# Optimization experiments

Measured on AMD Instinct MI355X. Metric: run time of the kernel, lower is better.

## Reference

```python
import jax, jax.numpy as jnp
import numpy as np

B, S, QD, KD, VD, OD = 8, 2048, 768, 768, 768, 512

def setup_inputs() -> dict:
    key = jax.random.key(0)
    ks = jax.random.split(key, 14)
    s_q = 1.0 / np.sqrt(QD)
    s_k = 1.0 / np.sqrt(KD)
    s_v = 1.0 / np.sqrt(VD)
    return {
        "query": jax.random.normal(ks[0], (B, S, QD), jnp.float32),
        "key": jax.random.normal(ks[1], (B, S, KD), jnp.float32),
        "value": jax.random.normal(ks[2], (B, S, VD), jnp.float32),
        "Wqr": jax.random.normal(ks[3], (QD, OD), jnp.float32) * s_q,
        "bqr": jnp.zeros((OD,), jnp.float32),
        "Wqi": jax.random.normal(ks[4], (QD, OD), jnp.float32) * s_q,
        "bqi": jnp.zeros((OD,), jnp.float32),
        "Wkr": jax.random.normal(ks[5], (KD, OD), jnp.float32) * s_k,
        "bkr": jnp.zeros((OD,), jnp.float32),
        "Wki": jax.random.normal(ks[6], (KD, OD), jnp.float32) * s_k,
        "bki": jnp.zeros((OD,), jnp.float32),
        "Wv": jax.random.normal(ks[7], (VD, OD), jnp.float32) * s_v,
        "bv": jnp.zeros((OD,), jnp.float32),
        "coherence_weight": jnp.asarray(1.0, jnp.float32),
    }

def reference(query, key, value, Wqr, bqr, Wqi, bqi, Wkr, bkr, Wki, bki, Wv, bv, coherence_weight):
    # Complex-valued projections (real/imag parts via separate linears)
    q_r = jnp.einsum("bsq,qo->bso", query, Wqr) + bqr
    q_i = jnp.einsum("bsq,qo->bso", query, Wqi) + bqi
    k_r = jnp.einsum("bsk,ko->bso", key, Wkr) + bkr
    k_i = jnp.einsum("bsk,ko->bso", key, Wki) + bki
    v = jnp.einsum("bsv,vo->bso", value, Wv) + bv
    # Complex QK^T: (q_r + i q_i)(k_r - i k_i)^T pieces, as in the torch code
    att_real = jnp.einsum("bso,bto->bst", q_r, k_r) + jnp.einsum("bso,bto->bst", q_i, k_i)
    att_imag = jnp.einsum("bso,bto->bst", q_i, k_r) - jnp.einsum("bso,bto->bst", q_r, k_i)
    att_mag = jnp.sqrt(att_real ** 2 + att_imag ** 2)
    scale = jnp.asarray(1.0 / np.sqrt(OD), att_mag.dtype)
    weights = jax.nn.softmax(att_mag * scale, axis=-1)  # [B,S,S]
    output = jnp.einsum("bst,bto->bso", weights, v)  # [B,S,OD]
    coherence = jnp.mean(att_imag ** 2) * coherence_weight
    return output, coherence
```

## Files before the change

### kernel.cpp

```cpp
#include <hip/hip_runtime.h>
#include <math.h>
#include <stdint.h>

#define S_    2048
#define SCALE_ 0.044194173824159216f

typedef __attribute__((ext_vector_type(8))) short short8;
typedef __attribute__((ext_vector_type(4))) float f32x4;

#define MFMA16(a, b, c) __builtin_amdgcn_mfma_f32_16x16x32_bf16((a), (b), (c), 0, 0, 0)

__device__ __forceinline__ void glds16(const void* g, void* l) {
  __builtin_amdgcn_global_load_lds(
      (const __attribute__((address_space(1))) void*)g,
      (__attribute__((address_space(3))) void*)l, 16, 0, 0);
}

__device__ __forceinline__ unsigned short f2bf(float f) {
  unsigned u = __float_as_uint(f);
  u += 0x7FFFu + ((u >> 16) & 1u);
  return (unsigned short)(u >> 16);
}

__global__ __launch_bounds__(256) void convert_kernel(
    const float* __restrict__ src, unsigned short* __restrict__ dst, int n4) {
  int i = blockIdx.x * 256 + threadIdx.x;
  if (i >= n4) return;
  float4 v = ((const float4*)src)[i];
  ushort4 o;
  o.x = f2bf(v.x); o.y = f2bf(v.y); o.z = f2bf(v.z); o.w = f2bf(v.w);
  ((ushort4*)dst)[i] = o;
}

__global__ void bias_build_kernel(const float* bqr, const float* bqi,
                                  const float* bkr, const float* bki,
                                  const float* bv, float* bq, float* bk,
                                  float* bvo) {
  int t = blockIdx.x * 256 + threadIdx.x;
  if (t < 512) { bq[t] = bqr[t]; bk[t] = bkr[t]; bvo[t] = bv[t]; }
  else if (t < 1024) { bq[t] = bqi[t - 512]; bk[t] = bki[t - 512]; }
}

__global__ __launch_bounds__(256) void wtrans_kernel(
    const float* __restrict__ W, unsigned short* __restrict__ Wt, int N,
    int row_off) {
  __shared__ float t[32][33];
  int n0 = blockIdx.x * 32, k0 = blockIdx.y * 32;
  int tx = threadIdx.x & 31, ty = threadIdx.x >> 5;
#pragma unroll
  for (int r = 0; r < 4; ++r)
    t[ty + r * 8][tx] = W[(size_t)(k0 + ty + r * 8) * N + n0 + tx];
  __syncthreads();
#pragma unroll
  for (int r = 0; r < 4; ++r)
    Wt[(size_t)(row_off + n0 + ty + r * 8) * 768 + k0 + tx] =
        f2bf(t[tx][ty + r * 8]);
}

__global__ void init_kernel(float* lsum, float* coh) {
  int t = blockIdx.x * 256 + threadIdx.x;
  if (t < 16384) lsum[t] = 0.f;
  if (t == 0) *coh = 0.f;
}

__global__ __launch_bounds__(256, 2) void proj_kernel(
    const unsigned short* __restrict__ Xb, const unsigned short* __restrict__ Wt,
    const float* __restrict__ bias, unsigned short* __restrict__ Y, int N,
    int vt_mode) {
  __shared__ char lds[32768];
  const int tid = threadIdx.x;
  const int lane = tid & 63, wid = tid >> 6;
  const int wi = wid >> 1, wj = wid & 1;
  const int m0 = blockIdx.y * 128, n0 = blockIdx.x * 128;
  const char* Xc = (const char*)Xb;
  const char* Wc = (const char*)Wt;

  f32x4 acc[4][4] = {};
  const int tile = wid >> 1;

  for (int s = 0; s < 12; ++s) {
    __syncthreads();
#pragma unroll
    for (int iss = 0; iss < 8; ++iss) {
      int gbase = wid * 512 + iss * 64;
      int loc = (gbase & 1023) + lane;
      int r = loc >> 3, blk = loc & 7;
      int sb = blk ^ (r & 7);
      const char* src = (tile == 0)
          ? Xc + (size_t)(m0 + r) * 1536 + s * 128 + sb * 16
          : Wc + (size_t)(n0 + r) * 1536 + s * 128 + sb * 16;
      glds16(src, lds + gbase * 16);
    }
    __syncthreads();
#pragma unroll
    for (int kk = 0; kk < 2; ++kk) {
      int blk = kk * 4 + (lane >> 4);
      short8 a[4];
#pragma unroll
      for (int i = 0; i < 4; ++i) {
        int row = wi * 64 + i * 16 + (lane & 15);
        a[i] = *(const short8*)(lds + row * 128 + ((blk ^ (row & 7)) << 4));
      }
#pragma unroll
      for (int j = 0; j < 4; ++j) {
        int row = wj * 64 + j * 16 + (lane & 15);
        short8 b = *(const short8*)(lds + 16384 + row * 128 +
                                    ((blk ^ (row & 7)) << 4));
#pragma unroll
        for (int i = 0; i < 4; ++i) acc[i][j] = MFMA16(a[i], b, acc[i][j]);
      }
    }
  }

#pragma unroll
  for (int j = 0; j < 4; ++j) {
    int n = n0 + wj * 64 + j * 16 + (lane & 15);
    float bn = bias[n];
    if (!vt_mode) {
#pragma unroll
      for (int i = 0; i < 4; ++i) {
        int mrow = m0 + wi * 64 + i * 16 + (lane >> 4) * 4;
#pragma unroll
        for (int r = 0; r < 4; ++r)
          Y[(size_t)(mrow + r) * N + n] = f2bf(acc[i][j][r] + bn);
      }
    } else {
#pragma unroll
      for (int i = 0; i < 4; ++i) {
        int mrow = m0 + wi * 64 + i * 16 + (lane >> 4) * 4;
        int b = mrow >> 11, key = mrow & 2047;
        ushort4 o;
        o.x = f2bf(acc[i][j][0] + bn);
        o.y = f2bf(acc[i][j][1] + bn);
        o.z = f2bf(acc[i][j][2] + bn);
        o.w = f2bf(acc[i][j][3] + bn);
        *(ushort4*)&Y[((size_t)b * 512 + n) * 2048 + key] = o;
      }
    }
  }
}

__global__ __launch_bounds__(256, 2) void score_kernel(
    const unsigned short* __restrict__ Qcat,
    const unsigned short* __restrict__ Kcat, unsigned short* __restrict__ P,
    float* __restrict__ lsum, float* __restrict__ coh) {
  __shared__ char lds[65536];
  const int tid = threadIdx.x;
  const int lane = tid & 63, wid = tid >> 6;
  const int wi = wid >> 1, wj = wid & 1;

  int id = blockIdx.x;
  int w = (id & 7) * 256 + (id >> 3);
  int batch = w >> 8;
  int tilein = w & 255;
  int q0 = (tilein >> 4) * 128;
  int k0 = (tilein & 15) * 128;

  const char* Qc = (const char*)Qcat + ((size_t)batch * 2048 + q0) * 2048;
  const char* Kc = (const char*)Kcat + ((size_t)batch * 2048 + k0) * 2048;

  f32x4 accre[4][4] = {}, accim[4][4] = {};
  const short sg = (short)0x8000;
  const short8 SGN = {sg, sg, sg, sg, sg, sg, sg, sg};

  const char* base = (wid < 2) ? Qc : Kc;
  const int hioff = (wid & 1) * 1024;

  for (int s = 0; s < 8; ++s) {
    __syncthreads();
#pragma unroll
    for (int iss = 0; iss < 16; ++iss) {
      int loc = iss * 64 + lane;
      int r = loc >> 3, blk = loc & 7;
      int sb = blk ^ (r & 7);
      glds16(base + (size_t)r * 2048 + s * 128 + hioff + sb * 16,
             lds + wid * 16384 + iss * 1024);
    }
    __syncthreads();
#pragma unroll
    for (int kk = 0; kk < 2; ++kk) {
      int blk = kk * 4 + (lane >> 4);
      short8 alo[4], ahi[4];
#pragma unroll
      for (int i = 0; i < 4; ++i) {
        int row = wi * 64 + i * 16 + (lane & 15);
        int sw = (blk ^ (row & 7)) << 4;
        alo[i] = *(const short8*)(lds + row * 128 + sw);
        ahi[i] = *(const short8*)(lds + 16384 + row * 128 + sw);
      }
#pragma unroll
      for (int j = 0; j < 4; ++j) {
        int row = wj * 64 + j * 16 + (lane & 15);
        int sw = (blk ^ (row & 7)) << 4;
        short8 blo = *(const short8*)(lds + 32768 + row * 128 + sw);
        short8 bhi = *(const short8*)(lds + 49152 + row * 128 + sw);
        short8 bhin = bhi ^ SGN;
#pragma unroll
        for (int i = 0; i < 4; ++i) {
          accre[i][j] = MFMA16(alo[i], blo, accre[i][j]);
          accre[i][j] = MFMA16(ahi[i], bhi, accre[i][j]);
          accim[i][j] = MFMA16(ahi[i], blo, accim[i][j]);
          accim[i][j] = MFMA16(alo[i], bhin, accim[i][j]);
        }
      }
    }
  }

  float csum = 0.f;
  size_t prow_base = (size_t)batch * 2048;
  float rsum[16];
#pragma unroll
  for (int t = 0; t < 16; ++t) rsum[t] = 0.f;

#pragma unroll
  for (int i = 0; i < 4; ++i) {
#pragma unroll
    for (int r = 0; r < 4; ++r) {
      int row = q0 + wi * 64 + i * 16 + (lane >> 4) * 4 + r;
      unsigned short* prow = P + (prow_base + row) * 2048;
      float rs = 0.f;
#pragma unroll
      for (int j = 0; j < 4; ++j) {
        float re = accre[i][j][r], im = accim[i][j][r];
        csum += im * im;
        float p = __expf(sqrtf(re * re + im * im) * SCALE_);
        rs += p;
        prow[k0 + wj * 64 + j * 16 + (lane & 15)] = f2bf(p);
      }
      rsum[i * 4 + r] = rs;
    }
  }
#pragma unroll
  for (int t = 0; t < 16; ++t) {
    float v = rsum[t];
    v += __shfl_xor(v, 1, 64);
    v += __shfl_xor(v, 2, 64);
    v += __shfl_xor(v, 4, 64);
    v += __shfl_xor(v, 8, 64);
    rsum[t] = v;
  }
  if ((lane & 15) == 0) {
#pragma unroll
    for (int i = 0; i < 4; ++i)
#pragma unroll
      for (int r = 0; r < 4; ++r) {
        int row = q0 + wi * 64 + i * 16 + (lane >> 4) * 4 + r;
        atomicAdd(&lsum[prow_base + row], rsum[i * 4 + r]);
      }
  }
#pragma unroll
  for (int m = 1; m < 64; m <<= 1) csum += __shfl_xor(csum, m, 64);
  __syncthreads();
  float* cred = (float*)lds;
  if (lane == 0) cred[wid] = csum;
  __syncthreads();
  if (tid == 0) atomicAdd(coh, cred[0] + cred[1] + cred[2] + cred[3]);
}

__global__ __launch_bounds__(256, 2) void pv_kernel(
    const unsigned short* __restrict__ P, const unsigned short* __restrict__ Vt,
    const float* __restrict__ lsum, float* __restrict__ out) {
  __shared__ char lds[32768];
  const int tid = threadIdx.x;
  const int lane = tid & 63, wid = tid >> 6;
  const int wi = wid >> 1, wj = wid & 1;

  int id = blockIdx.x;
  int w = (id & 7) * 64 + (id >> 3);
  int batch = w >> 6, tilein = w & 63;
  int i0 = (tilein >> 2) * 128;
  int o0 = (tilein & 3) * 128;

  const char* Pc = (const char*)P + (size_t)batch * 2048 * 4096;
  const char* Vc = (const char*)Vt + (size_t)batch * 512 * 4096;

  f32x4 acc[4][4] = {};
  const int tile = wid >> 1;

  for (int s = 0; s < 32; ++s) {
    __syncthreads();
#pragma unroll
    for (int iss = 0; iss < 8; ++iss) {
      int gbase = wid * 512 + iss * 64;
      int loc = (gbase & 1023) + lane;
      int r = loc >> 3, blk = loc & 7;
      int sb = blk ^ (r & 7);
      const char* src = (tile == 0)
          ? Pc + (size_t)(i0 + r) * 4096 + s * 128 + sb * 16
          : Vc + (size_t)(o0 + r) * 4096 + s * 128 + sb * 16;
      glds16(src, lds + gbase * 16);
    }
    __syncthreads();
#pragma unroll
    for (int kk = 0; kk < 2; ++kk) {
      int blk = kk * 4 + (lane >> 4);
      short8 a[4];
#pragma unroll
      for (int i = 0; i < 4; ++i) {
        int row = wi * 64 + i * 16 + (lane & 15);
        a[i] = *(const short8*)(lds + row * 128 + ((blk ^ (row & 7)) << 4));
      }
#pragma unroll
      for (int j = 0; j < 4; ++j) {
        int row = wj * 64 + j * 16 + (lane & 15);
        short8 b = *(const short8*)(lds + 16384 + row * 128 +
                                    ((blk ^ (row & 7)) << 4));
#pragma unroll
        for (int i = 0; i < 4; ++i) acc[i][j] = MFMA16(a[i], b, acc[i][j]);
      }
    }
  }

#pragma unroll
  for (int i = 0; i < 4; ++i) {
    int mrow = i0 + wi * 64 + i * 16 + (lane >> 4) * 4;
    float linv[4];
#pragma unroll
    for (int r = 0; r < 4; ++r)
      linv[r] = 1.0f / lsum[(size_t)batch * 2048 + mrow + r];
#pragma unroll
    for (int j = 0; j < 4; ++j) {
      int n = o0 + wj * 64 + j * 16 + (lane & 15);
#pragma unroll
      for (int r = 0; r < 4; ++r)
        out[((size_t)batch * 2048 + mrow + r) * 512 + n] = acc[i][j][r] * linv[r];
    }
  }
}

__global__ void finalize_kernel(const float* __restrict__ coh,
                                const float* __restrict__ cw,
                                float* __restrict__ out_last) {
  *out_last = (*coh) * (1.0f / 33554432.0f) * (*cw);
}

extern "C" void kernel_launch(void* const* d_in, const int* in_sizes, int n_in,
                              void* d_out, int out_size, void* d_ws,
                              size_t ws_size, hipStream_t stream) {
  const float* query = (const float*)d_in[0];
  const float* key   = (const float*)d_in[1];
  const float* value = (const float*)d_in[2];
  const float* Wqr = (const float*)d_in[3];
  const float* bqr = (const float*)d_in[4];
  const float* Wqi = (const float*)d_in[5];
  const float* bqi = (const float*)d_in[6];
  const float* Wkr = (const float*)d_in[7];
  const float* bkr = (const float*)d_in[8];
  const float* Wki = (const float*)d_in[9];
  const float* bki = (const float*)d_in[10];
  const float* Wv  = (const float*)d_in[11];
  const float* bv  = (const float*)d_in[12];
  const float* cw  = (const float*)d_in[13];
  float* out = (float*)d_out;

  char* ws = (char*)d_ws;
  unsigned short* XQ   = (unsigned short*)(ws + 0);
  unsigned short* XK   = (unsigned short*)(ws + 25165824);
  unsigned short* XV   = (unsigned short*)(ws + 50331648);
  unsigned short* Pbuf = (unsigned short*)(ws + 0);
  unsigned short* WTQ  = (unsigned short*)(ws + 75497472);
  unsigned short* WTK  = (unsigned short*)(ws + 77070336);
  unsigned short* WTV  = (unsigned short*)(ws + 78643200);
  float* BQ   = (float*)(ws + 79429632);
  float* BK   = (float*)(ws + 79433728);
  float* BV   = (float*)(ws + 79437824);
  unsigned short* QCAT = (unsigned short*)(ws + 79441920);
  unsigned short* KCAT = (unsigned short*)(ws + 112996352);
  unsigned short* VT   = (unsigned short*)(ws + 146550784);
  float* LSUM = (float*)(ws + 163328000);
  float* COH  = (float*)(ws + 163393536);
  if (ws_size < 163393600) return;

  convert_kernel<<<12288, 256, 0, stream>>>(query, XQ, 3145728);
  convert_kernel<<<12288, 256, 0, stream>>>(key, XK, 3145728);
  convert_kernel<<<12288, 256, 0, stream>>>(value, XV, 3145728);
  bias_build_kernel<<<4, 256, 0, stream>>>(bqr, bqi, bkr, bki, bv, BQ, BK, BV);
  wtrans_kernel<<<dim3(16, 24), 256, 0, stream>>>(Wqr, WTQ, 512, 0);
  wtrans_kernel<<<dim3(16, 24), 256, 0, stream>>>(Wqi, WTQ, 512, 512);
  wtrans_kernel<<<dim3(16, 24), 256, 0, stream>>>(Wkr, WTK, 512, 0);
  wtrans_kernel<<<dim3(16, 24), 256, 0, stream>>>(Wki, WTK, 512, 512);
  wtrans_kernel<<<dim3(16, 24), 256, 0, stream>>>(Wv, WTV, 512, 0);

  proj_kernel<<<dim3(8, 128), 256, 0, stream>>>(XQ, WTQ, BQ, QCAT, 1024, 0);
  proj_kernel<<<dim3(8, 128), 256, 0, stream>>>(XK, WTK, BK, KCAT, 1024, 0);
  proj_kernel<<<dim3(4, 128), 256, 0, stream>>>(XV, WTV, BV, VT, 512, 1);

  init_kernel<<<64, 256, 0, stream>>>(LSUM, COH);
  score_kernel<<<2048, 256, 0, stream>>>(QCAT, KCAT, Pbuf, LSUM, COH);
  pv_kernel<<<512, 256, 0, stream>>>(Pbuf, VT, LSUM, out);
  finalize_kernel<<<1, 1, 0, stream>>>(COH, cw, out + 8388608);
}
```

Measured before the change: 378.0 us.

## Pipeline score kernel with triple-buffered LDS, larger tiles, and fuse input converts

The score kernel moves to 512-thread blocks computing 256x128 tiles, with a three-stage LDS ring that prefetches K-slices two steps ahead. The prefetch loads are interleaved with the MFMA work, using explicit waitcnt, barriers and setprio. This targets the load/compute serialization of the old two-barrier loop and increases Q/K reuse per block. The three fp32-to-bf16 convert launches are merged into one. The cost is 144KB of LDS per block, which limits occupancy to one block per CU, plus more complex synchronization.

```diff
diff --git a/kernel.cpp b/kernel.cpp
--- a/kernel.cpp
+++ b/kernel.cpp
@@ -22,14 +22,19 @@
   return (unsigned short)(u >> 16);
 }
 
-__global__ __launch_bounds__(256) void convert_kernel(
-    const float* __restrict__ src, unsigned short* __restrict__ dst, int n4) {
+__global__ __launch_bounds__(256) void convert3_kernel(
+    const float* __restrict__ a, const float* __restrict__ b,
+    const float* __restrict__ c, unsigned short* __restrict__ oa,
+    unsigned short* __restrict__ ob, unsigned short* __restrict__ oc) {
   int i = blockIdx.x * 256 + threadIdx.x;
-  if (i >= n4) return;
-  float4 v = ((const float4*)src)[i];
+  int which = i / 3145728;
+  int off = i - which * 3145728;
+  const float* s = (which == 0) ? a : (which == 1) ? b : c;
+  unsigned short* d = (which == 0) ? oa : (which == 1) ? ob : oc;
+  float4 v = ((const float4*)s)[off];
   ushort4 o;
   o.x = f2bf(v.x); o.y = f2bf(v.y); o.z = f2bf(v.z); o.w = f2bf(v.w);
-  ((ushort4*)dst)[i] = o;
+  ((ushort4*)d)[off] = o;
 }
 
 __global__ void bias_build_kernel(const float* bqr, const float* bqi,
@@ -140,21 +145,24 @@
   }
 }
 
-__global__ __launch_bounds__(256, 2) void score_kernel(
+__global__ __launch_bounds__(512, 2) void score_kernel(
     const unsigned short* __restrict__ Qcat,
     const unsigned short* __restrict__ Kcat, unsigned short* __restrict__ P,
     float* __restrict__ lsum, float* __restrict__ coh) {
-  __shared__ char lds[65536];
+  __shared__ char lds[147456];
   const int tid = threadIdx.x;
   const int lane = tid & 63, wid = tid >> 6;
-  const int wi = wid >> 1, wj = wid & 1;
-
-  int id = blockIdx.x;
-  int w = (id & 7) * 256 + (id >> 3);
-  int batch = w >> 8;
-  int tilein = w & 255;
-  int q0 = (tilein >> 4) * 128;
-  int k0 = (tilein & 15) * 128;
+  const int wm = wid >> 1;
+  const int wn = wid & 1;
+  const int lr = lane & 15;
+  const int lk = lane >> 4;
+  const int l8 = lane >> 3, lb = lane & 7;
+
+  const int id = blockIdx.x;
+  const int batch = id & 7;
+  const int tile = id >> 3;
+  const int q0 = (tile >> 4) << 8;
+  const int k0 = (tile & 15) << 7;
 
   const char* Qc = (const char*)Qcat + ((size_t)batch * 2048 + q0) * 2048;
   const char* Kc = (const char*)Kcat + ((size_t)batch * 2048 + k0) * 2048;
@@ -163,60 +171,86 @@
   const short sg = (short)0x8000;
   const short8 SGN = {sg, sg, sg, sg, sg, sg, sg, sg};
 
-  const char* base = (wid < 2) ? Qc : Kc;
-  const int hioff = (wid & 1) * 1024;
-
-  for (int s = 0; s < 8; ++s) {
-    __syncthreads();
-#pragma unroll
-    for (int iss = 0; iss < 16; ++iss) {
-      int loc = iss * 64 + lane;
-      int r = loc >> 3, blk = loc & 7;
-      int sb = blk ^ (r & 7);
-      glds16(base + (size_t)r * 2048 + s * 128 + hioff + sb * 16,
-             lds + wid * 16384 + iss * 1024);
-    }
-    __syncthreads();
-#pragma unroll
-    for (int kk = 0; kk < 2; ++kk) {
-      int blk = kk * 4 + (lane >> 4);
-      short8 alo[4], ahi[4];
+  auto stage = [&](int t, char* setbase, int L) {
+    int row, sb;
+    const char* src;
+    if (L < 32) {
+      row = (L << 3) + l8;
+      sb = lb ^ (row & 7);
+      src = Qc + (size_t)row * 2048 + t * 64 + (sb & 3) * 16 + (sb >> 2) * 1024;
+    } else {
+      row = ((L - 32) << 3) + l8;
+      sb = lb ^ (row & 7);
+      src = Kc + (size_t)row * 2048 + t * 64 + (sb & 3) * 16 + (sb >> 2) * 1024;
+    }
+    glds16(src, setbase + (L << 10));
+  };
+
+#pragma unroll
+  for (int u = 0; u < 6; ++u) stage(0, lds, wid * 6 + u);
+#pragma unroll
+  for (int u = 0; u < 6; ++u) stage(1, lds + 49152, wid * 6 + u);
+  asm volatile("s_waitcnt vmcnt(6)" ::: "memory");
+  __builtin_amdgcn_s_barrier();
+
+  for (int t = 0; t < 16; ++t) {
+    char* rbase = lds + (t % 3) * 49152;
+    char* wbase = lds + ((t + 2) % 3) * 49152;
+    short8 alo[4], ahi[4];
+#pragma unroll
+    for (int j = 0; j < 4; ++j) {
+      if (j == 0) {
+#pragma unroll
+        for (int i = 0; i < 4; ++i) {
+          int ar = wm * 64 + i * 16 + lr;
+          const char* arow = rbase + ar * 128;
+          alo[i] = *(const short8*)(arow + ((lk ^ (ar & 7)) << 4));
+          ahi[i] = *(const short8*)(arow + (((4 + lk) ^ (ar & 7)) << 4));
+        }
+      }
+      int br = wn * 64 + j * 16 + lr;
+      const char* brow = rbase + 32768 + br * 128;
+      short8 blo = *(const short8*)(brow + ((lk ^ (br & 7)) << 4));
+      short8 bhi = *(const short8*)(brow + (((4 + lk) ^ (br & 7)) << 4));
+      if (t < 14) {
+        if (j == 0)      { stage(t + 2, wbase, wid * 6 + 0); stage(t + 2, wbase, wid * 6 + 1); }
+        else if (j == 1) { stage(t + 2, wbase, wid * 6 + 2); stage(t + 2, wbase, wid * 6 + 3); }
+        else if (j == 2) { stage(t + 2, wbase, wid * 6 + 4); }
+        else             { stage(t + 2, wbase, wid * 6 + 5); }
+      }
+      __builtin_amdgcn_s_barrier();
+      asm volatile("s_waitcnt lgkmcnt(0)" ::: "memory");
+      __builtin_amdgcn_sched_barrier(0);
+      __builtin_amdgcn_s_setprio(1);
+      short8 bhin = bhi ^ SGN;
 #pragma unroll
       for (int i = 0; i < 4; ++i) {
-        int row = wi * 64 + i * 16 + (lane & 15);
-        int sw = (blk ^ (row & 7)) << 4;
-        alo[i] = *(const short8*)(lds + row * 128 + sw);
-        ahi[i] = *(const short8*)(lds + 16384 + row * 128 + sw);
-      }
-#pragma unroll
-      for (int j = 0; j < 4; ++j) {
-        int row = wj * 64 + j * 16 + (lane & 15);
-        int sw = (blk ^ (row & 7)) << 4;
-        short8 blo = *(const short8*)(lds + 32768 + row * 128 + sw);
-        short8 bhi = *(const short8*)(lds + 49152 + row * 128 + sw);
-        short8 bhin = bhi ^ SGN;
-#pragma unroll
-        for (int i = 0; i < 4; ++i) {
-          accre[i][j] = MFMA16(alo[i], blo, accre[i][j]);
-          accre[i][j] = MFMA16(ahi[i], bhi, accre[i][j]);
-          accim[i][j] = MFMA16(ahi[i], blo, accim[i][j]);
-          accim[i][j] = MFMA16(alo[i], bhin, accim[i][j]);
-        }
-      }
-    }
-  }
+        accre[i][j] = MFMA16(alo[i], blo, accre[i][j]);
+        accre[i][j] = MFMA16(ahi[i], bhi, accre[i][j]);
+        accim[i][j] = MFMA16(ahi[i], blo, accim[i][j]);
+        accim[i][j] = MFMA16(alo[i], bhin, accim[i][j]);
+      }
+      __builtin_amdgcn_s_setprio(0);
+      if (j == 3) {
+        if (t < 14)       asm volatile("s_waitcnt vmcnt(6)" ::: "memory");
+        else if (t == 14) asm volatile("s_waitcnt vmcnt(0)" ::: "memory");
+      }
+      __builtin_amdgcn_s_barrier();
+    }
+  }
+  __syncthreads();
 
   float csum = 0.f;
   size_t prow_base = (size_t)batch * 2048;
   float rsum[16];
 #pragma unroll
-  for (int t = 0; t < 16; ++t) rsum[t] = 0.f;
+  for (int x = 0; x < 16; ++x) rsum[x] = 0.f;
 
 #pragma unroll
   for (int i = 0; i < 4; ++i) {
 #pragma unroll
     for (int r = 0; r < 4; ++r) {
-      int row = q0 + wi * 64 + i * 16 + (lane >> 4) * 4 + r;
+      int row = q0 + wm * 64 + i * 16 + lk * 4 + r;
       unsigned short* prow = P + (prow_base + row) * 2048;
       float rs = 0.f;
 #pragma unroll
@@ -225,36 +259,40 @@
         csum += im * im;
         float p = __expf(sqrtf(re * re + im * im) * SCALE_);
         rs += p;
-        prow[k0 + wj * 64 + j * 16 + (lane & 15)] = f2bf(p);
+        prow[k0 + wn * 64 + j * 16 + lr] = f2bf(p);
       }
       rsum[i * 4 + r] = rs;
     }
   }
 #pragma unroll
-  for (int t = 0; t < 16; ++t) {
-    float v = rsum[t];
+  for (int x = 0; x < 16; ++x) {
+    float v = rsum[x];
     v += __shfl_xor(v, 1, 64);
     v += __shfl_xor(v, 2, 64);
     v += __shfl_xor(v, 4, 64);
     v += __shfl_xor(v, 8, 64);
-    rsum[t] = v;
-  }
-  if ((lane & 15) == 0) {
+    rsum[x] = v;
+  }
+  if (lr == 0) {
 #pragma unroll
     for (int i = 0; i < 4; ++i)
 #pragma unroll
       for (int r = 0; r < 4; ++r) {
-        int row = q0 + wi * 64 + i * 16 + (lane >> 4) * 4 + r;
+        int row = q0 + wm * 64 + i * 16 + lk * 4 + r;
         atomicAdd(&lsum[prow_base + row], rsum[i * 4 + r]);
       }
   }
 #pragma unroll
   for (int m = 1; m < 64; m <<= 1) csum += __shfl_xor(csum, m, 64);
-  __syncthreads();
   float* cred = (float*)lds;
   if (lane == 0) cred[wid] = csum;
   __syncthreads();
-  if (tid == 0) atomicAdd(coh, cred[0] + cred[1] + cred[2] + cred[3]);
+  if (tid == 0) {
+    float s = 0.f;
+#pragma unroll
+    for (int w = 0; w < 8; ++w) s += cred[w];
+    atomicAdd(coh, s);
+  }
 }
 
 __global__ __launch_bounds__(256, 2) void pv_kernel(
@@ -371,9 +409,7 @@
   float* COH  = (float*)(ws + 163393536);
   if (ws_size < 163393600) return;
 
-  convert_kernel<<<12288, 256, 0, stream>>>(query, XQ, 3145728);
-  convert_kernel<<<12288, 256, 0, stream>>>(key, XK, 3145728);
-  convert_kernel<<<12288, 256, 0, stream>>>(value, XV, 3145728);
+  convert3_kernel<<<36864, 256, 0, stream>>>(query, key, value, XQ, XK, XV);
   bias_build_kernel<<<4, 256, 0, stream>>>(bqr, bqi, bkr, bki, bv, BQ, BK, BV);
   wtrans_kernel<<<dim3(16, 24), 256, 0, stream>>>(Wqr, WTQ, 512, 0);
   wtrans_kernel<<<dim3(16, 24), 256, 0, stream>>>(Wqi, WTQ, 512, 512);
@@ -386,7 +422,7 @@
   proj_kernel<<<dim3(4, 128), 256, 0, stream>>>(XV, WTV, BV, VT, 512, 1);
 
   init_kernel<<<64, 256, 0, stream>>>(LSUM, COH);
-  score_kernel<<<2048, 256, 0, stream>>>(QCAT, KCAT, Pbuf, LSUM, COH);
+  score_kernel<<<1024, 512, 0, stream>>>(QCAT, KCAT, Pbuf, LSUM, COH);
   pv_kernel<<<512, 256, 0, stream>>>(Pbuf, VT, LSUM, out);
   finalize_kernel<<<1, 1, 0, stream>>>(COH, cw, out + 8388608);
 }
```

New measurement: 383.3 us. No clear change (+1.4%).
